# Kernel optimization log

Hardware: AMD Instinct MI355X
Metric: run time of the kernel (lower is better)

## Reference

```python
import jax, jax.numpy as jnp
import numpy as np

L, T, D = 3, 65536, 256


def setup_inputs() -> dict:
    key = jax.random.key(0)
    ks = jax.random.split(key, 10)
    stdv = 1.0 / np.sqrt(D)
    u = lambda k, shape: jax.random.uniform(k, shape, jnp.float32, -stdv, stdv)
    return {
        "story": jax.random.normal(ks[0], (T, D), jnp.float32),
        "question": jax.random.normal(ks[1], (D,), jnp.float32),
        "Wz_f": u(ks[2], (L, D, D)),
        "bz_f": u(ks[3], (L, D)),
        "Wh_f": u(ks[4], (L, 2 * D, D)),
        "bh_f": u(ks[5], (L, D)),
        "Wz_b": u(ks[6], (L, D, D)),
        "bz_b": u(ks[7], (L, D)),
        "Wh_b": u(ks[8], (L, 2 * D, D)),
        "bh_b": u(ks[9], (L, D)),
    }


def _qrn_dir(x, q, Wz, bz, Wh, bh):
    """One QRN layer in one direction. x, q: [T, D]. Returns h states [T, D]."""
    z = jax.nn.sigmoid((x * q) @ Wz + bz)                      # [T, D]
    h_tilde = jnp.tanh(jnp.concatenate([x, q], axis=-1) @ Wh + bh)  # [T, D]
    a = 1.0 - z            # multiplicative factor on h_prev
    b = z * h_tilde        # additive term
    # linear recurrence h_t = a_t * h_{t-1} + b_t, h_0 = 0 -> associative scan
    def comb(c1, c2):
        a1, b1 = c1
        a2, b2 = c2
        return a1 * a2, a2 * b1 + b2
    _, h = jax.lax.associative_scan(comb, (a, b), axis=0)
    return h  # h[t] = hidden state after statement t


def reference(story, question, Wz_f, bz_f, Wh_f, bh_f, Wz_b, bz_b, Wh_b, bh_b):
    q = jnp.broadcast_to(question, story.shape)  # layer-0 question per step
    for layer in range(L):
        h_fwd = _qrn_dir(story, q, Wz_f[layer], bz_f[layer], Wh_f[layer], bh_f[layer])
        # backward direction: reversed story with correspondingly reversed questions
        h_bwd_rev = _qrn_dir(story[::-1], q[::-1], Wz_b[layer], bz_b[layer],
                             Wh_b[layer], bh_b[layer])
        if layer < L - 1:
            # q_{t}^{k+1} = h_fwd_t + h_bwd_t (aligned back to forward order)
            q = h_fwd + h_bwd_rev[::-1]
    return h_fwd[-1]  # final forward hidden state of last layer, [D]
```

## Files before the change

### kernel.cpp

```cpp
#include <hip/hip_runtime.h>
#include <hip/hip_bf16.h>
#include <math.h>

#define D    256
#define BT   128
#define GN   128
#define NSEG 32

typedef unsigned short u16;
typedef unsigned int   u32;
typedef __attribute__((ext_vector_type(8))) short short8;
typedef __attribute__((ext_vector_type(4))) float floatx4;

__device__ __forceinline__ float b2f(u16 v) {
    union { unsigned u; float f; } x; x.u = ((unsigned)v) << 16; return x.f;
}
__device__ __forceinline__ u16 f2b(float f) {
    union { unsigned u; float f; } x; x.f = f;
    unsigned lsb = (x.u >> 16) & 1;
    x.u += 0x7fffu + lsb;
    return (u16)(x.u >> 16);
}
__device__ __forceinline__ float sigm(float x) {
    return __builtin_amdgcn_rcpf(1.0f + __expf(-x));
}
__device__ __forceinline__ float tanhfast(float x) {
    return 1.0f - 2.0f * __builtin_amdgcn_rcpf(__expf(2.0f * x) + 1.0f);
}
__device__ __forceinline__ void async16(const u16* g, u16* l) {
    __builtin_amdgcn_global_load_lds(
        (const __attribute__((address_space(1))) unsigned int*)g,
        (__attribute__((address_space(3))) unsigned int*)l, 16, 0, 0);
}

__global__ __launch_bounds__(256) void wtrans_kernel(
    const float* __restrict__ question,
    const float* __restrict__ Wz_f, const float* __restrict__ Wh_f,
    const float* __restrict__ Wz_b, const float* __restrict__ Wh_b,
    u16* __restrict__ wt)
{
    int id = blockIdx.x * 256 + threadIdx.x;
    int combo = id / (3 * 65536);
    int rem   = id % (3 * 65536);
    int m = rem >> 16;
    int e = rem & 65535;
    int k = e >> 8, n = e & 255;
    int l   = combo < 3 ? combo : combo - 3;
    int dir = combo < 3 ? 0 : 1;
    float v;
    if (m == 0) {
        const float* Wz = dir ? Wz_b : Wz_f;
        v = Wz[((size_t)l * D + k) * D + n];
        if (l == 0) v *= question[k];
    } else {
        const float* Wh = dir ? Wh_b : Wh_f;
        int kk = (m == 2) ? (k + D) : k;
        v = Wh[((size_t)l * 2 * D + kk) * D + n];
    }
    wt[(size_t)combo * 3 * 65536 + (size_t)m * 65536 + (size_t)n * D + k] = f2b(v);
}

__global__ __launch_bounds__(256) void bias0_kernel(
    const float* __restrict__ question,
    const float* __restrict__ Wh_f, const float* __restrict__ Wh_b,
    const float* __restrict__ bh_f, const float* __restrict__ bh_b,
    float* __restrict__ bh0f, float* __restrict__ bh0b)
{
    const float* Wh = blockIdx.x ? Wh_b : Wh_f;
    const float* bh = blockIdx.x ? bh_b : bh_f;
    float* out = blockIdx.x ? bh0b : bh0f;
    int n = threadIdx.x;
    float acc = bh[n];
    for (int k = 0; k < D; ++k)
        acc = fmaf(question[k], Wh[(size_t)(D + k) * D + n], acc);
    out[n] = acc;
}

__global__ __launch_bounds__(256) void prep0_kernel(
    const float* __restrict__ story, u16* __restrict__ xb)
{
    long id = (long)blockIdx.x * 256 + threadIdx.x;
    const float* xp = story + id * 8;
    float4 xa = *(const float4*)xp;
    float4 xc = *(const float4*)(xp + 4);
    float xv[8] = {xa.x, xa.y, xa.z, xa.w, xc.x, xc.y, xc.z, xc.w};
    short8 xs;
    #pragma unroll
    for (int i = 0; i < 8; ++i) xs[i] = (short)f2b(xv[i]);
    *(short8*)(xb + id * 8) = xs;
}

struct StageS {
    u16 ax [BT * 32]; u16 aq [BT * 32]; u16 axq[BT * 32];
    u16 bz_[GN * 32]; u16 bx_[GN * 32]; u16 bq_[GN * 32];
};
struct Stage0 {
    u16 ax [BT * 32]; u16 bz_[GN * 32]; u16 bx_[GN * 32];
};
struct EpiP  { float segA[NSEG][GN]; float segB[NSEG][GN]; };
union __align__(16) SharedP  { StageS st; EpiP ep; };
union __align__(16) SharedP0 { Stage0 st; EpiP ep; };

__device__ __forceinline__ void gate_epilogue(
    EpiP& ep, int tid, int t0, int n0,
    floatx4 (&accz)[4][2], floatx4 (&acch)[4][2],
    const float* bz, const float* bh,
    float* aggA, float* aggB, u32* abg, int FWD)
{
    const int lane = tid & 63, w = tid >> 6;
    const int wr = w & 1, wc = w >> 1;
    const int lr = lane & 15, quad = lane >> 4;

    float bzn[2], bhn[2];
    #pragma unroll
    for (int ct = 0; ct < 2; ++ct) {
        int n = n0 + wc * 32 + ct * 16 + lr;
        bzn[ct] = bz[n]; bhn[ct] = bh[n];
    }
    float av[4][2][4], bvv[4][2][4];
    #pragma unroll
    for (int rt = 0; rt < 4; ++rt) {
        #pragma unroll
        for (int ct = 0; ct < 2; ++ct) {
            #pragma unroll
            for (int r = 0; r < 4; ++r) {
                float z  = sigm(accz[rt][ct][r] + bzn[ct]);
                float ht = tanhfast(acch[rt][ct][r] + bhn[ct]);
                av[rt][ct][r]  = 1.0f - z;
                bvv[rt][ct][r] = z * ht;
            }
            float A = 1.f, B = 0.f;
            if (FWD) {
                #pragma unroll
                for (int r = 0; r < 4; ++r) { A = av[rt][ct][r] * A; B = fmaf(av[rt][ct][r], B, bvv[rt][ct][r]); }
            } else {
                #pragma unroll
                for (int r = 3; r >= 0; --r) { A = av[rt][ct][r] * A; B = fmaf(av[rt][ct][r], B, bvv[rt][ct][r]); }
            }
            int seg = wr * 16 + rt * 4 + quad;
            int col = wc * 32 + ct * 16 + lr;
            ep.segA[seg][col] = A;
            ep.segB[seg][col] = B;
        }
    }
    __syncthreads();

    if (tid < GN) {
        float A = 1.f, B = 0.f;
        if (FWD) {
            #pragma unroll
            for (int sg = 0; sg < NSEG; ++sg) {
                float a = ep.segA[sg][tid], b = ep.segB[sg][tid];
                ep.segA[sg][tid] = A; ep.segB[sg][tid] = B;
                A = a * A; B = fmaf(a, B, b);
            }
        } else {
            #pragma unroll
            for (int sg = NSEG - 1; sg >= 0; --sg) {
                float a = ep.segA[sg][tid], b = ep.segB[sg][tid];
                ep.segA[sg][tid] = A; ep.segB[sg][tid] = B;
                A = a * A; B = fmaf(a, B, b);
            }
        }
        int c = t0 / BT;
        aggA[(size_t)c * D + n0 + tid] = A;
        aggB[(size_t)c * D + n0 + tid] = B;
    }

    if (abg) {
        __syncthreads();
        #pragma unroll
        for (int rt = 0; rt < 4; ++rt) {
            #pragma unroll
            for (int ct = 0; ct < 2; ++ct) {
                int seg = wr * 16 + rt * 4 + quad;
                int col = wc * 32 + ct * 16 + lr;
                float Pa = ep.segA[seg][col];
                float Pb = ep.segB[seg][col];
                size_t base = (size_t)(t0 + wr * 64 + rt * 16 + quad * 4) * D + n0 + col;
                if (FWD) {
                    #pragma unroll
                    for (int r = 0; r < 4; ++r) {
                        Pa = av[rt][ct][r] * Pa;
                        Pb = fmaf(av[rt][ct][r], Pb, bvv[rt][ct][r]);
                        abg[base + (size_t)r * D] = (u32)f2b(Pa) | ((u32)f2b(Pb) << 16);
                    }
                } else {
                    #pragma unroll
                    for (int r = 3; r >= 0; --r) {
                        Pa = av[rt][ct][r] * Pa;
                        Pb = fmaf(av[rt][ct][r], Pb, bvv[rt][ct][r]);
                        abg[base + (size_t)r * D] = (u32)f2b(Pa) | ((u32)f2b(Pb) << 16);
                    }
                }
            }
        }
    }
}

__device__ __forceinline__ void gemm_body(
    SharedP& sh, int tid, int c, int n0,
    const u16* xbg, const u16* qg, const u16* xqg, const u16* wt,
    const float* bz, const float* bh,
    float* aggA, float* aggB, u32* abg, int FWD)
{
    const int t0   = c * BT;
    const int lane = tid & 63, w = tid >> 6;
    const int wr = w & 1, wc = w >> 1;
    const int lr   = lane & 15, quad = lane >> 4;

    const int swA   = (quad ^ ((lr >> 1) & 3)) * 8;
    const int offA0 = (wr * 64 + lr) * 32 + swA;
    const int offB0 = (wc * 32 + lr) * 32 + swA;

    floatx4 accz[4][2], acch[4][2];
    #pragma unroll
    for (int rt = 0; rt < 4; ++rt)
        #pragma unroll
        for (int ct = 0; ct < 2; ++ct) {
            accz[rt][ct] = (floatx4){0.f,0.f,0.f,0.f};
            acch[rt][ct] = (floatx4){0.f,0.f,0.f,0.f};
        }

    const int lb = (tid & ~63) * 8;

    const int arow = tid >> 2;
    const int agg_ = (tid & 3) ^ ((arow >> 1) & 3);
    const size_t goA = (size_t)(t0 + arow) * D + agg_ * 8;
    const size_t goB = (size_t)(n0 + arow) * D + agg_ * 8;
    const u16* pax  = xbg + goA;
    const u16* paq  = qg  + goA;
    const u16* paxq = xqg + goA;
    const u16* pbz  = wt + goB;
    const u16* pbx  = wt + 65536  + goB;
    const u16* pbq  = wt + 131072 + goB;

    #pragma unroll
    for (int k0 = 0; k0 < D; k0 += 32) {
        async16(pax  + k0, sh.st.ax  + lb);
        async16(paq  + k0, sh.st.aq  + lb);
        async16(paxq + k0, sh.st.axq + lb);
        async16(pbz  + k0, sh.st.bz_ + lb);
        async16(pbx  + k0, sh.st.bx_ + lb);
        async16(pbq  + k0, sh.st.bq_ + lb);
        __syncthreads();

        short8 vz[2], vx[2], vq[2];
        #pragma unroll
        for (int ct = 0; ct < 2; ++ct) {
            vz[ct] = *(const short8*)(sh.st.bz_ + offB0 + ct * 512);
            vx[ct] = *(const short8*)(sh.st.bx_ + offB0 + ct * 512);
            vq[ct] = *(const short8*)(sh.st.bq_ + offB0 + ct * 512);
        }
        #pragma unroll
        for (int rt = 0; rt < 4; ++rt) {
            short8 fxq = *(const short8*)(sh.st.axq + offA0 + rt * 512);
            short8 fx  = *(const short8*)(sh.st.ax  + offA0 + rt * 512);
            short8 fq  = *(const short8*)(sh.st.aq  + offA0 + rt * 512);
            #pragma unroll
            for (int ct = 0; ct < 2; ++ct) {
                accz[rt][ct] = __builtin_amdgcn_mfma_f32_16x16x32_bf16(fxq, vz[ct], accz[rt][ct], 0, 0, 0);
                acch[rt][ct] = __builtin_amdgcn_mfma_f32_16x16x32_bf16(fx , vx[ct], acch[rt][ct], 0, 0, 0);
                acch[rt][ct] = __builtin_amdgcn_mfma_f32_16x16x32_bf16(fq , vq[ct], acch[rt][ct], 0, 0, 0);
            }
        }
        __syncthreads();
    }

    gate_epilogue(sh.ep, tid, t0, n0, accz, acch, bz, bh, aggA, aggB, abg, FWD);
}

__device__ __forceinline__ void gemm0_body(
    SharedP0& sh, int tid, int c, int n0,
    const u16* xbg, const u16* wt,
    const float* bz, const float* bh0,
    float* aggA, float* aggB, u32* abg, int FWD)
{
    const int t0   = c * BT;
    const int lane = tid & 63, w = tid >> 6;
    const int wr = w & 1, wc = w >> 1;
    const int lr   = lane & 15, quad = lane >> 4;

    const int swA   = (quad ^ ((lr >> 1) & 3)) * 8;
    const int offA0 = (wr * 64 + lr) * 32 + swA;
    const int offB0 = (wc * 32 + lr) * 32 + swA;

    floatx4 accz[4][2], acch[4][2];
    #pragma unroll
    for (int rt = 0; rt < 4; ++rt)
        #pragma unroll
        for (int ct = 0; ct < 2; ++ct) {
            accz[rt][ct] = (floatx4){0.f,0.f,0.f,0.f};
            acch[rt][ct] = (floatx4){0.f,0.f,0.f,0.f};
        }

    const int lb = (tid & ~63) * 8;
    const int arow = tid >> 2;
    const int agg_ = (tid & 3) ^ ((arow >> 1) & 3);
    const size_t goA = (size_t)(t0 + arow) * D + agg_ * 8;
    const size_t goB = (size_t)(n0 + arow) * D + agg_ * 8;
    const u16* pax = xbg + goA;
    const u16* pbz = wt + goB;
    const u16* pbx = wt + 65536 + goB;

    #pragma unroll
    for (int k0 = 0; k0 < D; k0 += 32) {
        async16(pax + k0, sh.st.ax  + lb);
        async16(pbz + k0, sh.st.bz_ + lb);
        async16(pbx + k0, sh.st.bx_ + lb);
        __syncthreads();

        short8 vz[2], vx[2];
        #pragma unroll
        for (int ct = 0; ct < 2; ++ct) {
            vz[ct] = *(const short8*)(sh.st.bz_ + offB0 + ct * 512);
            vx[ct] = *(const short8*)(sh.st.bx_ + offB0 + ct * 512);
        }
        #pragma unroll
        for (int rt = 0; rt < 4; ++rt) {
            short8 fx = *(const short8*)(sh.st.ax + offA0 + rt * 512);
            #pragma unroll
            for (int ct = 0; ct < 2; ++ct) {
                accz[rt][ct] = __builtin_amdgcn_mfma_f32_16x16x32_bf16(fx, vz[ct], accz[rt][ct], 0, 0, 0);
                acch[rt][ct] = __builtin_amdgcn_mfma_f32_16x16x32_bf16(fx, vx[ct], acch[rt][ct], 0, 0, 0);
            }
        }
        __syncthreads();
    }

    gate_epilogue(sh.ep, tid, t0, n0, accz, acch, bz, bh0, aggA, aggB, abg, FWD);
}

template<int FWD, int ABOUT>
__global__ __launch_bounds__(512, 4) void qrn_g5(
    const u16* __restrict__ xbg, const u16* __restrict__ qg,
    const u16* __restrict__ xqg, const u16* __restrict__ wt,
    const float* __restrict__ bz, const float* __restrict__ bh,
    float* __restrict__ aggA, float* __restrict__ aggB,
    u32* __restrict__ abg)
{
    __shared__ SharedP sh;
    const int tid  = threadIdx.x;
    const int bid  = (int)blockIdx.x;
    const int gidx = (bid & 7) * 128 + (bid >> 3);
    gemm_body(sh, tid, gidx >> 1, (gidx & 1) * GN,
              xbg, qg, xqg, wt, bz, bh, aggA, aggB, ABOUT ? abg : nullptr, FWD);
}

__global__ __launch_bounds__(512, 4) void qrn_gboth(
    const u16* __restrict__ xbg, const u16* __restrict__ qg,
    const u16* __restrict__ xqg,
    const u16* __restrict__ wtF, const u16* __restrict__ wtB,
    const float* __restrict__ bzf, const float* __restrict__ bhf,
    const float* __restrict__ bzb, const float* __restrict__ bhb,
    float* __restrict__ aggAf, float* __restrict__ aggBf,
    float* __restrict__ aggAb, float* __restrict__ aggBb,
    u32* __restrict__ abf, u32* __restrict__ abb)
{
    __shared__ SharedP sh;
    const int tid  = threadIdx.x;
    const int half = (int)blockIdx.x >> 10;
    const int bid  = (int)blockIdx.x & 1023;
    const int gidx = (bid & 7) * 128 + (bid >> 3);
    gemm_body(sh, tid, gidx >> 1, (gidx & 1) * GN,
              xbg, qg, xqg,
              half ? wtB : wtF,
              half ? bzb : bzf, half ? bhb : bhf,
              half ? aggAb : aggAf, half ? aggBb : aggBf,
              half ? abb : abf, half ? 0 : 1);
}

template<int FWD>
__global__ __launch_bounds__(512, 4) void qrn_g0(
    const u16* __restrict__ xbg, const u16* __restrict__ wt,
    const float* __restrict__ bz, const float* __restrict__ bh0,
    float* __restrict__ aggA, float* __restrict__ aggB,
    u32* __restrict__ abg)
{
    __shared__ SharedP0 sh;
    const int tid  = threadIdx.x;
    const int bid  = (int)blockIdx.x;
    const int gidx = (bid & 7) * 128 + (bid >> 3);
    gemm0_body(sh, tid, gidx >> 1, (gidx & 1) * GN,
               xbg, wt, bz, bh0, aggA, aggB, abg, FWD);
}

__global__ __launch_bounds__(512, 4) void qrn_g0both(
    const u16* __restrict__ xbg,
    const u16* __restrict__ wtF, const u16* __restrict__ wtB,
    const float* __restrict__ bzf, const float* __restrict__ bh0f,
    const float* __restrict__ bzb, const float* __restrict__ bh0b,
    float* __restrict__ aggAf, float* __restrict__ aggBf,
    float* __restrict__ aggAb, float* __restrict__ aggBb,
    u32* __restrict__ abf, u32* __restrict__ abb)
{
    __shared__ SharedP0 sh;
    const int tid  = threadIdx.x;
    const int half = (int)blockIdx.x >> 10;
    const int bid  = (int)blockIdx.x & 1023;
    const int gidx = (bid & 7) * 128 + (bid >> 3);
    gemm0_body(sh, tid, gidx >> 1, (gidx & 1) * GN,
               xbg,
               half ? wtB : wtF,
               half ? bzb : bzf, half ? bh0b : bh0f,
               half ? aggAb : aggAf, half ? aggBb : aggBf,
               half ? abb : abf, half ? 0 : 1);
}

__global__ __launch_bounds__(256) void replay2_fb(
    const u32* __restrict__ abf, const u32* __restrict__ abb,
    const float* __restrict__ hinif, const float* __restrict__ hinib,
    const u16* __restrict__ xb, u16* __restrict__ qout, u16* __restrict__ xq,
    int total8)
{
    for (int id = (int)blockIdx.x * 256 + (int)threadIdx.x; id < total8;
         id += (int)gridDim.x * 256) {
        int t  = id >> 5;
        int n0 = (id & 31) * 8;
        int c  = t >> 7;
        size_t o  = (size_t)t * D + n0;
        size_t hc = (size_t)c * D + n0;
        uint4 f0 = *(const uint4*)(abf + o);
        uint4 f1 = *(const uint4*)(abf + o + 4);
        uint4 g0 = *(const uint4*)(abb + o);
        uint4 g1 = *(const uint4*)(abb + o + 4);
        float4 hf0 = *(const float4*)(hinif + hc);
        float4 hf1 = *(const float4*)(hinif + hc + 4);
        float4 hb0 = *(const float4*)(hinib + hc);
        float4 hb1 = *(const float4*)(hinib + hc + 4);
        short8 xv = *(const short8*)(xb + o);
        u32 fa[8] = {f0.x, f0.y, f0.z, f0.w, f1.x, f1.y, f1.z, f1.w};
        u32 ga[8] = {g0.x, g0.y, g0.z, g0.w, g1.x, g1.y, g1.z, g1.w};
        float hfv[8] = {hf0.x, hf0.y, hf0.z, hf0.w, hf1.x, hf1.y, hf1.z, hf1.w};
        float hbv[8] = {hb0.x, hb0.y, hb0.z, hb0.w, hb1.x, hb1.y, hb1.z, hb1.w};
        short8 qs, xqs;
        #pragma unroll
        for (int i = 0; i < 8; ++i) {
            float hF = fmaf(b2f((u16)(fa[i] & 0xffff)), hfv[i], b2f((u16)(fa[i] >> 16)));
            float hB = fmaf(b2f((u16)(ga[i] & 0xffff)), hbv[i], b2f((u16)(ga[i] >> 16)));
            u16 qb = f2b(hF + hB);
            qs[i]  = (short)qb;
            xqs[i] = (short)f2b(b2f((u16)xv[i]) * b2f(qb));
        }
        *(short8*)(qout + o) = qs;
        *(short8*)(xq + o)   = xqs;
    }
}

__global__ __launch_bounds__(256) void replay2_f(
    const u32* __restrict__ abg, const float* __restrict__ hini,
    u16* __restrict__ qout, int total8)
{
    for (int id = (int)blockIdx.x * 256 + (int)threadIdx.x; id < total8;
         id += (int)gridDim.x * 256) {
        int t  = id >> 5;
        int n0 = (id & 31) * 8;
        int c  = t >> 7;
        size_t o  = (size_t)t * D + n0;
        size_t hc = (size_t)c * D + n0;
        uint4 f0 = *(const uint4*)(abg + o);
        uint4 f1 = *(const uint4*)(abg + o + 4);
        float4 hf0 = *(const float4*)(hini + hc);
        float4 hf1 = *(const float4*)(hini + hc + 4);
        u32 fa[8] = {f0.x, f0.y, f0.z, f0.w, f1.x, f1.y, f1.z, f1.w};
        float hfv[8] = {hf0.x, hf0.y, hf0.z, hf0.w, hf1.x, hf1.y, hf1.z, hf1.w};
        short8 qs;
        #pragma unroll
        for (int i = 0; i < 8; ++i) {
            float hF = fmaf(b2f((u16)(fa[i] & 0xffff)), hfv[i], b2f((u16)(fa[i] >> 16)));
            qs[i] = (short)f2b(hF);
        }
        *(short8*)(qout + o) = qs;
    }
}

__global__ __launch_bounds__(256) void replay2_b(
    const u32* __restrict__ abg, const float* __restrict__ hini,
    const u16* __restrict__ xb, u16* __restrict__ qout, u16* __restrict__ xq,
    int total8)
{
    for (int id = (int)blockIdx.x * 256 + (int)threadIdx.x; id < total8;
         id += (int)gridDim.x * 256) {
        int t  = id >> 5;
        int n0 = (id & 31) * 8;
        int c  = t >> 7;
        size_t o  = (size_t)t * D + n0;
        size_t hc = (size_t)c * D + n0;
        uint4 g0 = *(const uint4*)(abg + o);
        uint4 g1 = *(const uint4*)(abg + o + 4);
        float4 hb0 = *(const float4*)(hini + hc);
        float4 hb1 = *(const float4*)(hini + hc + 4);
        short8 qold = *(const short8*)(qout + o);
        short8 xv   = *(const short8*)(xb + o);
        u32 ga[8] = {g0.x, g0.y, g0.z, g0.w, g1.x, g1.y, g1.z, g1.w};
        float hbv[8] = {hb0.x, hb0.y, hb0.z, hb0.w, hb1.x, hb1.y, hb1.z, hb1.w};
        short8 qs, xqs;
        #pragma unroll
        for (int i = 0; i < 8; ++i) {
            float hB = fmaf(b2f((u16)(ga[i] & 0xffff)), hbv[i], b2f((u16)(ga[i] >> 16)));
            float qn = b2f((u16)qold[i]) + hB;
            u16 qb = f2b(qn);
            qs[i]  = (short)qb;
            xqs[i] = (short)f2b(b2f((u16)xv[i]) * b2f(qb));
        }
        *(short8*)(qout + o) = qs;
        *(short8*)(xq + o)   = xqs;
    }
}

__device__ __forceinline__ void scan_body(
    const float* aggA, const float* aggB, float* hinit, float* out_final,
    int fwd, int nch, int n, int tid)
{
    __shared__ float sA[256], sB[256];
    const int per = nch >> 8;
    float lA[4], lB[4];
    float A = 1.f, B = 0.f;
    for (int j = 0; j < per; ++j) {
        int pidx = tid * per + j;
        int c = fwd ? pidx : (nch - 1 - pidx);
        float a = aggA[(size_t)c * D + n];
        float b = aggB[(size_t)c * D + n];
        lA[j] = a; lB[j] = b;
        A = a * A;
        B = fmaf(a, B, b);
    }
    sA[tid] = A; sB[tid] = B;
    __syncthreads();
    for (int off = 1; off < 256; off <<= 1) {
        float pA = 1.f, pB = 0.f;
        if (tid >= off) { pA = sA[tid - off]; pB = sB[tid - off]; }
        __syncthreads();
        if (tid >= off) {
            float cA = sA[tid], cB = sB[tid];
            sA[tid] = pA * cA;
            sB[tid] = fmaf(cA, pB, cB);
        }
        __syncthreads();
    }
    float eB = (tid > 0) ? sB[tid - 1] : 0.f;
    for (int j = 0; j < per; ++j) {
        int pidx = tid * per + j;
        int c = fwd ? pidx : (nch - 1 - pidx);
        hinit[(size_t)c * D + n] = eB;
        eB = fmaf(lA[j], eB, lB[j]);
    }
    if (out_final != nullptr && tid == 0) out_final[n] = sB[255];
}

__global__ __launch_bounds__(256) void scan_p2_kernel(
    const float* __restrict__ aggA, const float* __restrict__ aggB,
    float* __restrict__ hinit, float* __restrict__ out_final, int fwd, int nch)
{
    scan_body(aggA, aggB, hinit, out_final, fwd, nch, blockIdx.x, threadIdx.x);
}

__global__ __launch_bounds__(256) void scan_dual_kernel(
    const float* __restrict__ aggAf, const float* __restrict__ aggBf, float* __restrict__ hf,
    const float* __restrict__ aggAb, const float* __restrict__ aggBb, float* __restrict__ hb,
    int nch)
{
    int b = blockIdx.x;
    int fwd = (b < D) ? 1 : 0;
    int n = fwd ? b : (b - D);
    scan_body(fwd ? aggAf : aggAb, fwd ? aggBf : aggBb,
              fwd ? hf : hb, nullptr, fwd, nch, n, threadIdx.x);
}

extern "C" void kernel_launch(void* const* d_in, const int* in_sizes, int n_in,
                              void* d_out, int out_size, void* d_ws, size_t ws_size,
                              hipStream_t stream) {
    const float* story    = (const float*)d_in[0];
    const float* question = (const float*)d_in[1];
    const float* Wz_f = (const float*)d_in[2];
    const float* bz_f = (const float*)d_in[3];
    const float* Wh_f = (const float*)d_in[4];
    const float* bh_f = (const float*)d_in[5];
    const float* Wz_b = (const float*)d_in[6];
    const float* bz_b = (const float*)d_in[7];
    const float* Wh_b = (const float*)d_in[8];
    const float* bh_b = (const float*)d_in[9];

    const int T    = in_sizes[0] / D;
    const int NCH  = T / BT;
    const size_t TD = (size_t)T * D;
    const size_t WTE = 5 * 3 * 65536;
    const int total8 = T * 32;

    const size_t needF = 3 * TD * 2 + WTE * 2 + 2 * TD * 4
                       + (size_t)4 * NCH * D * 4 + 2 * D * 4 + 4096;
    const bool planF = ws_size >= needF;

    dim3 blk(256);
    dim3 gblk(512);
    dim3 gGrid((unsigned)(NCH * 2));
    dim3 g2Grid((unsigned)(NCH * 4));
    dim3 rGrid(2048);
    dim3 pGrid((unsigned)(TD / 8 / 256));

    if (planF) {
        u16* xb = (u16*)d_ws;
        u16* q  = xb + TD;
        u16* xq = q  + TD;
        u16* wt = xq + TD;
        u32* abf = (u32*)(wt + WTE);
        u32* abb = abf + TD;
        float* aggAf = (float*)(abb + TD);
        float* aggBf = aggAf + (size_t)NCH * D;
        float* aggAb = aggBf + (size_t)NCH * D;
        float* aggBb = aggAb + (size_t)NCH * D;
        float* bh0f  = aggBb + (size_t)NCH * D;
        float* bh0b  = bh0f + D;
        float* hinif = aggBf;
        float* hinib = aggBb;

        wtrans_kernel<<<dim3(5 * 3 * 65536 / 256), blk, 0, stream>>>(
            question, Wz_f, Wh_f, Wz_b, Wh_b, wt);
        bias0_kernel<<<dim3(2), blk, 0, stream>>>(
            question, Wh_f, Wh_b, bh_f, bh_b, bh0f, bh0b);
        prep0_kernel<<<pGrid, blk, 0, stream>>>(story, xb);

        for (int l = 0; l < 3; ++l) {
            const u16*   wtf = wt + (size_t)l * 3 * 65536;
            const float* bzf = bz_f + (size_t)l * D;
            const float* bhf = bh_f + (size_t)l * D;

            if (l == 2) {
                qrn_g5<1,0><<<gGrid, gblk, 0, stream>>>(
                    xb, q, xq, wtf, bzf, bhf, aggAf, aggBf, nullptr);
                scan_p2_kernel<<<dim3(D), blk, 0, stream>>>(
                    aggAf, aggBf, hinif, (float*)d_out, 1, NCH);
                break;
            }
            const u16*   wtb = wt + (size_t)(3 + l) * 3 * 65536;
            const float* bzb = bz_b + (size_t)l * D;
            const float* bhb = bh_b + (size_t)l * D;

            if (l == 0) {
                qrn_g0both<<<g2Grid, gblk, 0, stream>>>(
                    xb, wtf, wtb, bzf, bh0f, bzb, bh0b,
                    aggAf, aggBf, aggAb, aggBb, abf, abb);
            } else {
                qrn_gboth<<<g2Grid, gblk, 0, stream>>>(
                    xb, q, xq, wtf, wtb, bzf, bhf, bzb, bhb,
                    aggAf, aggBf, aggAb, aggBb, abf, abb);
            }
            scan_dual_kernel<<<dim3(2 * D), blk, 0, stream>>>(
                aggAf, aggBf, hinif, aggAb, aggBb, hinib, NCH);
            replay2_fb<<<rGrid, blk, 0, stream>>>(
                abf, abb, hinif, hinib, xb, q, xq, total8);
        }
    } else {
        u16* xb = (u16*)d_ws;
        u16* qA = xb + TD;
        u16* qB = qA + TD;
        u16* xq = qB + TD;
        u16* wt = xq + TD;
        u32*   ab   = (u32*)(wt + WTE);
        float* aggA = (float*)(ab + TD);
        float* aggB = aggA + (size_t)NCH * D;
        float* bh0f = aggB + (size_t)NCH * D;
        float* bh0b = bh0f + D;
        float* hini = aggB;

        wtrans_kernel<<<dim3(5 * 3 * 65536 / 256), blk, 0, stream>>>(
            question, Wz_f, Wh_f, Wz_b, Wh_b, wt);
        bias0_kernel<<<dim3(2), blk, 0, stream>>>(
            question, Wh_f, Wh_b, bh_f, bh_b, bh0f, bh0b);
        prep0_kernel<<<pGrid, blk, 0, stream>>>(story, xb);

        const u16* qcur  = qA;
        u16*       qnext = qB;

        for (int l = 0; l < 3; ++l) {
            const u16*   wtf = wt + (size_t)l * 3 * 65536;
            const float* bzf = bz_f + (size_t)l * D;
            const float* bhf = bh_f + (size_t)l * D;

            if (l == 2) {
                qrn_g5<1,0><<<gGrid, gblk, 0, stream>>>(
                    xb, qcur, xq, wtf, bzf, bhf, aggA, aggB, nullptr);
                scan_p2_kernel<<<dim3(D), blk, 0, stream>>>(
                    aggA, aggB, hini, (float*)d_out, 1, NCH);
                break;
            }
            const u16*   wtb = wt + (size_t)(3 + l) * 3 * 65536;
            const float* bzb = bz_b + (size_t)l * D;
            const float* bhb = bh_b + (size_t)l * D;

            if (l == 0) {
                qrn_g0<1><<<gGrid, gblk, 0, stream>>>(
                    xb, wtf, bzf, bh0f, aggA, aggB, ab);
                scan_p2_kernel<<<dim3(D), blk, 0, stream>>>(aggA, aggB, hini, nullptr, 1, NCH);
                replay2_f<<<rGrid, blk, 0, stream>>>(ab, hini, qnext, total8);

                qrn_g0<0><<<gGrid, gblk, 0, stream>>>(
                    xb, wtb, bzb, bh0b, aggA, aggB, ab);
                scan_p2_kernel<<<dim3(D), blk, 0, stream>>>(aggA, aggB, hini, nullptr, 0, NCH);
                replay2_b<<<rGrid, blk, 0, stream>>>(ab, hini, xb, qnext, xq, total8);
            } else {
                qrn_g5<1,1><<<gGrid, gblk, 0, stream>>>(
                    xb, qcur, xq, wtf, bzf, bhf, aggA, aggB, ab);
                scan_p2_kernel<<<dim3(D), blk, 0, stream>>>(aggA, aggB, hini, nullptr, 1, NCH);
                replay2_f<<<rGrid, blk, 0, stream>>>(ab, hini, qnext, total8);

                qrn_g5<0,1><<<gGrid, gblk, 0, stream>>>(
                    xb, qcur, xq, wtb, bzb, bhb, aggA, aggB, ab);
                scan_p2_kernel<<<dim3(D), blk, 0, stream>>>(aggA, aggB, hini, nullptr, 0, NCH);
                replay2_b<<<rGrid, blk, 0, stream>>>(ab, hini, xb, qnext, xq, total8);
            }
            const u16* ts = qcur; qcur = qnext; qnext = (u16*)ts;
        }
    }
}
```

Baseline: 439.4 us.

## Double-buffer A tiles with async prefetch and explicit vmcnt waits in GEMM loops

```diff
diff --git a/kernel.cpp b/kernel.cpp
--- a/kernel.cpp
+++ b/kernel.cpp
@@ -91,11 +91,12 @@
 }
 
 struct StageS {
-    u16 ax [BT * 32]; u16 aq [BT * 32]; u16 axq[BT * 32];
+    u16 ax [2][BT * 32]; u16 aq [2][BT * 32]; u16 axq[2][BT * 32];
     u16 bz_[GN * 32]; u16 bx_[GN * 32]; u16 bq_[GN * 32];
 };
 struct Stage0 {
-    u16 ax [BT * 32]; u16 bz_[GN * 32]; u16 bx_[GN * 32];
+    u16 ax [2][BT * 32];
+    u16 bz_[GN * 32]; u16 bx_[GN * 32];
 };
 struct EpiP  { float segA[NSEG][GN]; float segB[NSEG][GN]; };
 union __align__(16) SharedP  { StageS st; EpiP ep; };
@@ -235,15 +236,27 @@
     const u16* pbx  = wt + 65536  + goB;
     const u16* pbq  = wt + 131072 + goB;
 
+    async16(pax , sh.st.ax [0] + lb);
+    async16(paq , sh.st.aq [0] + lb);
+    async16(paxq, sh.st.axq[0] + lb);
+
     #pragma unroll
-    for (int k0 = 0; k0 < D; k0 += 32) {
-        async16(pax  + k0, sh.st.ax  + lb);
-        async16(paq  + k0, sh.st.aq  + lb);
-        async16(paxq + k0, sh.st.axq + lb);
-        async16(pbz  + k0, sh.st.bz_ + lb);
-        async16(pbx  + k0, sh.st.bx_ + lb);
-        async16(pbq  + k0, sh.st.bq_ + lb);
-        __syncthreads();
+    for (int kk = 0; kk < 8; ++kk) {
+        const int cur = kk & 1, nxt = cur ^ 1;
+        const int k0 = kk * 32;
+        async16(pbz + k0, sh.st.bz_ + lb);
+        async16(pbx + k0, sh.st.bx_ + lb);
+        async16(pbq + k0, sh.st.bq_ + lb);
+        if (kk < 7) {
+            async16(pax  + k0 + 32, sh.st.ax [nxt] + lb);
+            async16(paq  + k0 + 32, sh.st.aq [nxt] + lb);
+            async16(paxq + k0 + 32, sh.st.axq[nxt] + lb);
+            asm volatile("s_waitcnt vmcnt(3)" ::: "memory");
+        } else {
+            asm volatile("s_waitcnt vmcnt(0)" ::: "memory");
+        }
+        __builtin_amdgcn_s_barrier();
+        asm volatile("" ::: "memory");
 
         short8 vz[2], vx[2], vq[2];
         #pragma unroll
@@ -254,9 +267,9 @@
         }
         #pragma unroll
         for (int rt = 0; rt < 4; ++rt) {
-            short8 fxq = *(const short8*)(sh.st.axq + offA0 + rt * 512);
-            short8 fx  = *(const short8*)(sh.st.ax  + offA0 + rt * 512);
-            short8 fq  = *(const short8*)(sh.st.aq  + offA0 + rt * 512);
+            short8 fxq = *(const short8*)(sh.st.axq[cur] + offA0 + rt * 512);
+            short8 fx  = *(const short8*)(sh.st.ax [cur] + offA0 + rt * 512);
+            short8 fq  = *(const short8*)(sh.st.aq [cur] + offA0 + rt * 512);
             #pragma unroll
             for (int ct = 0; ct < 2; ++ct) {
                 accz[rt][ct] = __builtin_amdgcn_mfma_f32_16x16x32_bf16(fxq, vz[ct], accz[rt][ct], 0, 0, 0);
@@ -264,7 +277,9 @@
                 acch[rt][ct] = __builtin_amdgcn_mfma_f32_16x16x32_bf16(fq , vq[ct], acch[rt][ct], 0, 0, 0);
             }
         }
-        __syncthreads();
+        asm volatile("" ::: "memory");
+        __builtin_amdgcn_s_barrier();
+        asm volatile("" ::: "memory");
     }
 
     gate_epilogue(sh.ep, tid, t0, n0, accz, acch, bz, bh, aggA, aggB, abg, FWD);
@@ -303,12 +318,22 @@
     const u16* pbz = wt + goB;
     const u16* pbx = wt + 65536 + goB;
 
+    async16(pax, sh.st.ax[0] + lb);
+
     #pragma unroll
-    for (int k0 = 0; k0 < D; k0 += 32) {
-        async16(pax + k0, sh.st.ax  + lb);
+    for (int kk = 0; kk < 8; ++kk) {
+        const int cur = kk & 1, nxt = cur ^ 1;
+        const int k0 = kk * 32;
         async16(pbz + k0, sh.st.bz_ + lb);
         async16(pbx + k0, sh.st.bx_ + lb);
-        __syncthreads();
+        if (kk < 7) {
+            async16(pax + k0 + 32, sh.st.ax[nxt] + lb);
+            asm volatile("s_waitcnt vmcnt(1)" ::: "memory");
+        } else {
+            asm volatile("s_waitcnt vmcnt(0)" ::: "memory");
+        }
+        __builtin_amdgcn_s_barrier();
+        asm volatile("" ::: "memory");
 
         short8 vz[2], vx[2];
         #pragma unroll
@@ -318,14 +343,16 @@
         }
         #pragma unroll
         for (int rt = 0; rt < 4; ++rt) {
-            short8 fx = *(const short8*)(sh.st.ax + offA0 + rt * 512);
+            short8 fx = *(const short8*)(sh.st.ax[cur] + offA0 + rt * 512);
             #pragma unroll
             for (int ct = 0; ct < 2; ++ct) {
                 accz[rt][ct] = __builtin_amdgcn_mfma_f32_16x16x32_bf16(fx, vz[ct], accz[rt][ct], 0, 0, 0);
                 acch[rt][ct] = __builtin_amdgcn_mfma_f32_16x16x32_bf16(fx, vx[ct], acch[rt][ct], 0, 0, 0);
             }
         }
-        __syncthreads();
+        asm volatile("" ::: "memory");
+        __builtin_amdgcn_s_barrier();
+        asm volatile("" ::: "memory");
     }
 
     gate_epilogue(sh.ep, tid, t0, n0, accz, acch, bz, bh0, aggA, aggB, abg, FWD);
```

Result: faster. 413.9 us (-5.8%).
